# Kernel optimization log

Hardware: AMD Instinct MI355X
Metric: run time of the kernel (lower is better)

Reference implementation:

```python
import jax, jax.numpy as jnp
import numpy as np

M0, M1 = 16, 16          # n_modes
C = 64                   # hidden_channels
B = 16                   # batch
H = W = 128              # spatial resolution
SCALE = C ** (-2)        # matches torch: scale * torch.rand(...)


def setup_inputs() -> dict:
    key = jax.random.key(0)
    kx, k0r, k0i, k1r, k1i = jax.random.split(key, 5)
    X = jax.random.normal(kx, (B, C, H, W), dtype=jnp.float32)
    wshape = (C, C, M0, M1)
    # torch.rand with cfloat draws U[0,1) for real and imag parts independently
    w0r = SCALE * jax.random.uniform(k0r, wshape, dtype=jnp.float32)
    w0i = SCALE * jax.random.uniform(k0i, wshape, dtype=jnp.float32)
    w1r = SCALE * jax.random.uniform(k1r, wshape, dtype=jnp.float32)
    w1i = SCALE * jax.random.uniform(k1i, wshape, dtype=jnp.float32)
    return {"X": X, "w0r": w0r, "w0i": w0i, "w1r": w1r, "w1i": w1i}


def reference(X, w0r, w0i, w1r, w1i):
    w0 = w0r + 1j * w0i                       # linear0: (C, C, M0, M1) complex
    w1 = w1r + 1j * w1i                       # linear1
    Xf = jnp.fft.rfftn(X, axes=(-2, -1), norm="forward")   # (B, C, H, W//2+1) complex
    # out[b,c] = sum_t weight[c,t] * Xf[b,t] on the two kept-mode corners
    top = jnp.einsum("ctxy,btxy->bcxy", w0, Xf[:, :, :M0, :M1])
    bot = jnp.einsum("ctxy,btxy->bcxy", w1, Xf[:, :, -M0:, :M1])
    Y = jnp.zeros_like(Xf)
    Y = Y.at[:, :, :M0, :M1].set(top)
    Y = Y.at[:, :, -M0:, :M1].set(bot)
    out = jnp.fft.irfftn(Y, axes=(-2, -1), s=(H, W), norm="forward")
    return out.astype(jnp.float32)
```

## Files before the change

kernel.cpp:

```cpp
#include <hip/hip_runtime.h>

#define PI2 6.28318530717958647692f

__global__ __launch_bounds__(256, 4) void k_fwd(const float* __restrict__ X,
                                                float* __restrict__ Xf) {
  __shared__ __attribute__((aligned(16))) float A2t[128 * 18 * 2];
  __shared__ __attribute__((aligned(16))) float Tt[64 * 16 * 2];
  const int plane = blockIdx.x;
  const int tid = threadIdx.x;
  const float* Xp = X + (size_t)plane * (128 * 128);

  #pragma unroll
  for (int k = 0; k < 4; ++k) {
    int idx = tid + k * 256;
    int h = idx >> 4, slot = idx & 15;
    int kx = slot ? slot : 16;
    float ang = -PI2 * (float)((kx * h) & 127) / 128.f;
    float s_, c_;
    __sincosf(ang, &s_, &c_);
    Tt[idx * 2] = c_; Tt[idx * 2 + 1] = s_;
  }
  __syncthreads();

  {
    const int w2 = tid & 63;
    const int kxq = tid >> 6;
    float ar[4][2], ai[4][2];
    #pragma unroll
    for (int j = 0; j < 4; ++j) {
      ar[j][0] = 0.f; ar[j][1] = 0.f; ai[j][0] = 0.f; ai[j][1] = 0.f;
    }
    float dcA = 0.f, dcB = 0.f;
    float x0a = Xp[w2],      x1a = Xp[64 * 128 + w2];
    float x0b = Xp[w2 + 64], x1b = Xp[64 * 128 + w2 + 64];
    for (int h = 0; h < 64; ++h) {
      float n0a = 0.f, n1a = 0.f, n0b = 0.f, n1b = 0.f;
      if (h < 63) {
        n0a = Xp[(h + 1) * 128 + w2];      n1a = Xp[(h + 65) * 128 + w2];
        n0b = Xp[(h + 1) * 128 + w2 + 64]; n1b = Xp[(h + 65) * 128 + w2 + 64];
      }
      float uea = x0a + x1a, uoa = x0a - x1a;
      float ueb = x0b + x1b, uob = x0b - x1b;
      const float4* Trow = (const float4*)&Tt[h * 32];
      float4 e01 = Trow[kxq * 2];
      float4 e23 = Trow[kxq * 2 + 1];
      ar[0][0] = fmaf(uea, e01.x, ar[0][0]); ai[0][0] = fmaf(uea, e01.y, ai[0][0]);
      ar[0][1] = fmaf(ueb, e01.x, ar[0][1]); ai[0][1] = fmaf(ueb, e01.y, ai[0][1]);
      ar[1][0] = fmaf(uoa, e01.z, ar[1][0]); ai[1][0] = fmaf(uoa, e01.w, ai[1][0]);
      ar[1][1] = fmaf(uob, e01.z, ar[1][1]); ai[1][1] = fmaf(uob, e01.w, ai[1][1]);
      ar[2][0] = fmaf(uea, e23.x, ar[2][0]); ai[2][0] = fmaf(uea, e23.y, ai[2][0]);
      ar[2][1] = fmaf(ueb, e23.x, ar[2][1]); ai[2][1] = fmaf(ueb, e23.y, ai[2][1]);
      ar[3][0] = fmaf(uoa, e23.z, ar[3][0]); ai[3][0] = fmaf(uoa, e23.w, ai[3][0]);
      ar[3][1] = fmaf(uob, e23.z, ar[3][1]); ai[3][1] = fmaf(uob, e23.w, ai[3][1]);
      if (kxq == 0) { dcA += uea; dcB += ueb; }
      x0a = n0a; x1a = n1a; x0b = n0b; x1b = n1b;
    }
    #pragma unroll
    for (int j = 0; j < 4; ++j) {
      int s = kxq * 4 + j;
      int row = (s == 0) ? 16 : s;
      *(float2*)&A2t[(w2 * 18 + row) * 2]        = make_float2(ar[j][0], ai[j][0]);
      *(float2*)&A2t[((w2 + 64) * 18 + row) * 2] = make_float2(ar[j][1], ai[j][1]);
    }
    if (kxq == 0) {
      *(float2*)&A2t[(w2 * 18) * 2]        = make_float2(dcA, 0.f);
      *(float2*)&A2t[((w2 + 64) * 18) * 2] = make_float2(dcB, 0.f);
    }
  }
  __syncthreads();

  {
    const int kxi = tid >> 3;
    const int t = tid & 7;
    const int row = (kxi < 16) ? kxi : (32 - kxi);
    const float csign = (kxi < 16) ? 1.f : -1.f;
    const float s = (t & 1) ? -1.f : 1.f;
    float s0r, s0i, s1r, s1i;
    __sincosf(-PI2 * (float)t / 128.f, &s0i, &s0r);
    __sincosf(-PI2 * (float)(t + 8) / 128.f, &s1i, &s1r);
    float r0 = 0.f, i0 = 0.f, r1 = 0.f, i1 = 0.f;
    float E0r = 1.f, E0i = 0.f, E1r = 1.f, E1i = 0.f;
    #pragma unroll
    for (int half = 0; half < 2; ++half) {
      if (half == 1) {
        float c_, s_;
        __sincosf(-1.57079632679489662f * (float)t, &s_, &c_);
        E0r = c_; E0i = s_; E1r = c_; E1i = s_;
      }
      for (int w = half * 32; w < half * 32 + 32; ++w) {
        float2 a = *(const float2*)&A2t[(w * 18 + row) * 2];
        float2 b = *(const float2*)&A2t[((w + 64) * 18 + row) * 2];
        float ur = fmaf(s, b.x, a.x);
        float ui = csign * fmaf(s, b.y, a.y);
        r0 = fmaf(ur, E0r, r0); r0 = fmaf(-ui, E0i, r0);
        i0 = fmaf(ur, E0i, i0); i0 = fmaf(ui, E0r, i0);
        r1 = fmaf(ur, E1r, r1); r1 = fmaf(-ui, E1i, r1);
        i1 = fmaf(ur, E1i, i1); i1 = fmaf(ui, E1r, i1);
        float u0 = E0r * s0r - E0i * s0i; E0i = E0r * s0i + E0i * s0r; E0r = u0;
        float u1 = E1r * s1r - E1i * s1i; E1i = E1r * s1i + E1i * s1r; E1r = u1;
      }
    }
    const float sc = 1.f / 16384.f;
    float* base = Xf + (size_t)plane * 1024 + kxi * 32;
    *(float2*)&base[t * 2]       = make_float2(r0 * sc, i0 * sc);
    *(float2*)&base[(t + 8) * 2] = make_float2(r1 * sc, i1 * sc);
  }
}

__global__ __launch_bounds__(256, 2) void k_mix(const float* __restrict__ Xf,
                                                const float* __restrict__ w0r,
                                                const float* __restrict__ w0i,
                                                const float* __restrict__ w1r,
                                                const float* __restrict__ w1i,
                                                float* __restrict__ Y) {
  __shared__ __attribute__((aligned(16))) float Wl[4 * 32 * 16 * 4];
  const int bid = blockIdx.x;
  const int c2 = bid >> 8;
  const int x  = (bid >> 4) & 15;
  const int cg = bid & 15;
  const int c0 = cg * 4;
  const int kxi = c2 * 16 + x;
  const float* Wr_g = c2 ? w1r : w0r;
  const float* Wi_g = c2 ? w1i : w0i;
  const int tid = threadIdx.x;
  const int b = tid >> 4;
  const int y = tid & 15;

  #pragma unroll
  for (int k = 0; k < 16; ++k) {
    int idx = tid + k * 256;
    int y_ = idx & 15, t_ = (idx >> 4) & 63, c_ = idx >> 10;
    size_t ga = (((size_t)(c0 + c_) * 64 + t_) * 16 + x) * 16 + y_;
    int f2i = ((c_ * 32 + (t_ >> 1)) * 16 + y_) * 2 + (t_ & 1);
    *(float2*)&Wl[f2i * 2] = make_float2(Wr_g[ga], Wi_g[ga]);
  }
  __syncthreads();

  float aR[4] = {}, aI[4] = {};
  const float* xbase = Xf + ((size_t)b * 64) * 1024 + kxi * 32 + y * 2;
  for (int t8 = 0; t8 < 64; t8 += 8) {
    float2 xv[8];
    #pragma unroll
    for (int q = 0; q < 8; ++q)
      xv[q] = *(const float2*)&xbase[(size_t)(t8 + q) * 1024];
    #pragma unroll
    for (int p = 0; p < 4; ++p) {
      int t2 = (t8 >> 1) + p;
      float2 xe = xv[2 * p], xo = xv[2 * p + 1];
      #pragma unroll
      for (int cj = 0; cj < 4; ++cj) {
        float4 wv = *(const float4*)&Wl[((cj * 32 + t2) * 16 + y) * 4];
        aR[cj] = fmaf(xe.x, wv.x, aR[cj]); aR[cj] = fmaf(-xe.y, wv.y, aR[cj]);
        aI[cj] = fmaf(xe.x, wv.y, aI[cj]); aI[cj] = fmaf(xe.y, wv.x, aI[cj]);
        aR[cj] = fmaf(xo.x, wv.z, aR[cj]); aR[cj] = fmaf(-xo.y, wv.w, aR[cj]);
        aI[cj] = fmaf(xo.x, wv.w, aI[cj]); aI[cj] = fmaf(xo.y, wv.z, aI[cj]);
      }
    }
  }
  #pragma unroll
  for (int cj = 0; cj < 4; ++cj) {
    size_t ya = ((size_t)(b * 64 + c0 + cj)) * 1024 + kxi * 32 + y * 2;
    *(float2*)&Y[ya] = make_float2(aR[cj], aI[cj]);
  }
}

__global__ __launch_bounds__(256, 4) void k_inv(const float* __restrict__ Y,
                                                float* __restrict__ out) {
  __shared__ __attribute__((aligned(16))) float Yl[1024];
  __shared__ __attribute__((aligned(16))) float Mt[128 * 16 * 2];
  const int plane = blockIdx.x;
  const int tid = threadIdx.x;
  *(float4*)&Yl[tid * 4] = *(const float4*)&Y[(size_t)plane * 1024 + tid * 4];
  __syncthreads();

  {
    const int g = tid >> 6;
    const int h2 = tid & 63;
    float zr[2][4] = {}, zi[2][4] = {};
    float uw, uwi;
    __sincosf(PI2 * (float)h2 / 128.f, &uwi, &uw);
    const float4* Yl4 = (const float4*)Yl;
    float Tr = 1.f, Ti = 0.f;
    #pragma unroll 2
    for (int kxi = 0; kxi < 16; ++kxi) {
      float sgn = (kxi & 1) ? -1.f : 1.f;
      #pragma unroll
      for (int q = 0; q < 2; ++q) {
        float4 p = Yl4[kxi * 8 + g * 2 + q];
        float cr0 = p.x * Tr - p.y * Ti, ci0 = p.x * Ti + p.y * Tr;
        float cr1 = p.z * Tr - p.w * Ti, ci1 = p.z * Ti + p.w * Tr;
        zr[0][2*q]   += cr0; zi[0][2*q]   += ci0;
        zr[0][2*q+1] += cr1; zi[0][2*q+1] += ci1;
        zr[1][2*q]   = fmaf(sgn, cr0, zr[1][2*q]);   zi[1][2*q]   = fmaf(sgn, ci0, zi[1][2*q]);
        zr[1][2*q+1] = fmaf(sgn, cr1, zr[1][2*q+1]); zi[1][2*q+1] = fmaf(sgn, ci1, zi[1][2*q+1]);
      }
      float nr = Tr * uw - Ti * uwi, ni = Tr * uwi + Ti * uw;
      Tr = nr; Ti = ni;
    }
    __sincosf(PI2 * (float)((112 * h2) & 127) / 128.f, &Ti, &Tr);
    #pragma unroll 2
    for (int kxi = 16; kxi < 32; ++kxi) {
      float sgn = (kxi & 1) ? -1.f : 1.f;
      #pragma unroll
      for (int q = 0; q < 2; ++q) {
        float4 p = Yl4[kxi * 8 + g * 2 + q];
        float cr0 = p.x * Tr - p.y * Ti, ci0 = p.x * Ti + p.y * Tr;
        float cr1 = p.z * Tr - p.w * Ti, ci1 = p.z * Ti + p.w * Tr;
        zr[0][2*q]   += cr0; zi[0][2*q]   += ci0;
        zr[0][2*q+1] += cr1; zi[0][2*q+1] += ci1;
        zr[1][2*q]   = fmaf(sgn, cr0, zr[1][2*q]);   zi[1][2*q]   = fmaf(sgn, ci0, zi[1][2*q]);
        zr[1][2*q+1] = fmaf(sgn, cr1, zr[1][2*q+1]); zi[1][2*q+1] = fmaf(sgn, ci1, zi[1][2*q+1]);
      }
      float nr = Tr * uw - Ti * uwi, ni = Tr * uwi + Ti * uw;
      Tr = nr; Ti = ni;
    }
    #pragma unroll
    for (int hs = 0; hs < 2; ++hs) {
      int h = h2 + hs * 64;
      #pragma unroll
      for (int q = 0; q < 2; ++q) {
        int ky0 = g * 4 + 2 * q;
        float f0 = (ky0 == 0) ? 1.f : 2.f;
        float4 v = make_float4(f0 * zr[hs][2*q],   -f0 * zi[hs][2*q],
                               2.f * zr[hs][2*q+1], -2.f * zi[hs][2*q+1]);
        int f4i = h * 8 + ((g * 2 + q) ^ (h & 7));
        *(float4*)&Mt[f4i * 4] = v;
      }
    }
  }
  __syncthreads();

  {
    const int hp = tid >> 5;
    const int w2 = tid & 31;
    float C[16], S[16];
    {
      float cw, sw;
      __sincosf(PI2 * (float)w2 / 128.f, &sw, &cw);
      C[0] = 1.f; S[0] = 0.f;
      #pragma unroll
      for (int k = 1; k < 16; ++k) {
        C[k] = C[k - 1] * cw - S[k - 1] * sw;
        S[k] = C[k - 1] * sw + S[k - 1] * cw;
      }
    }
    float* op = out + (size_t)plane * (128 * 128);
    const float4* Mt4 = (const float4*)Mt;
    #pragma unroll 2
    for (int hj = 0; hj < 16; ++hj) {
      int h = hp * 16 + hj;
      float e = 0.f, o = 0.f, e2 = 0.f, o2 = 0.f;
      #pragma unroll
      for (int j = 0; j < 8; ++j) {
        float4 m = Mt4[h * 8 + (j ^ (h & 7))];
        int k0 = 2 * j, k1 = 2 * j + 1;
        e = fmaf(m.x, C[k0], e); e = fmaf(m.y, S[k0], e);
        o = fmaf(m.z, C[k1], o); o = fmaf(m.w, S[k1], o);
        if ((k0 & 2) == 0) { e2 = fmaf(m.x, C[k0], e2); e2 = fmaf(m.y, S[k0], e2); }
        else               { e2 = fmaf(-m.x, C[k0], e2); e2 = fmaf(-m.y, S[k0], e2); }
        if ((k1 & 2) == 0) { o2 = fmaf(m.w, C[k1], o2); o2 = fmaf(-m.z, S[k1], o2); }
        else               { o2 = fmaf(-m.w, C[k1], o2); o2 = fmaf(m.z, S[k1], o2); }
      }
      op[h * 128 + w2]      = e + o;
      op[h * 128 + w2 + 64] = e - o;
      op[h * 128 + w2 + 32] = e2 + o2;
      op[h * 128 + w2 + 96] = e2 - o2;
    }
  }
}

extern "C" void kernel_launch(void* const* d_in, const int* in_sizes, int n_in,
                              void* d_out, int out_size, void* d_ws, size_t ws_size,
                              hipStream_t stream) {
  const float* X   = (const float*)d_in[0];
  const float* w0r = (const float*)d_in[1];
  const float* w0i = (const float*)d_in[2];
  const float* w1r = (const float*)d_in[3];
  const float* w1i = (const float*)d_in[4];
  float* outp = (float*)d_out;
  float* Xf = (float*)d_ws;
  float* Yw = (float*)d_ws + (1u << 20);
  k_fwd<<<1024, 256, 0, stream>>>(X, Xf);
  k_mix<<<512, 256, 0, stream>>>(Xf, w0r, w0i, w1r, w1i, Yw);
  k_inv<<<1024, 256, 0, stream>>>(Yw, outp);
}
```

Before: 165.7 us.

## Vectorize forward-column loads and split mix kernel across more blocks

In the forward kernel, each thread now reads two adjacent columns with float2 loads, two rows per iteration, so loads are wider and more are in flight. The mix kernel grid is doubled: each block handles half the batch, and each thread handles two output channels instead of four. Weight staging now uses float4 global loads that are interleaved into shared memory. The aim is more parallelism and better memory efficiency in the mix stage, at the cost of loading each block's weight slice twice across the two batch halves.

```diff
diff --git a/kernel.cpp b/kernel.cpp
--- a/kernel.cpp
+++ b/kernel.cpp
@@ -30,41 +30,54 @@
     for (int j = 0; j < 4; ++j) {
       ar[j][0] = 0.f; ar[j][1] = 0.f; ai[j][0] = 0.f; ai[j][1] = 0.f;
     }
-    float dcA = 0.f, dcB = 0.f;
-    float x0a = Xp[w2],      x1a = Xp[64 * 128 + w2];
-    float x0b = Xp[w2 + 64], x1b = Xp[64 * 128 + w2 + 64];
-    for (int h = 0; h < 64; ++h) {
-      float n0a = 0.f, n1a = 0.f, n0b = 0.f, n1b = 0.f;
-      if (h < 63) {
-        n0a = Xp[(h + 1) * 128 + w2];      n1a = Xp[(h + 65) * 128 + w2];
-        n0b = Xp[(h + 1) * 128 + w2 + 64]; n1b = Xp[(h + 65) * 128 + w2 + 64];
-      }
-      float uea = x0a + x1a, uoa = x0a - x1a;
-      float ueb = x0b + x1b, uob = x0b - x1b;
-      const float4* Trow = (const float4*)&Tt[h * 32];
+    float dc0 = 0.f, dc1 = 0.f;
+    const float* colp = Xp + 2 * w2;
+
+    float2 t0 = *(const float2*)&colp[0];
+    float2 b0 = *(const float2*)&colp[64 * 128];
+    float2 t1 = *(const float2*)&colp[128];
+    float2 b1 = *(const float2*)&colp[65 * 128];
+
+    auto rowstep = [&](int hh, float2 tt, float2 bb) {
+      float uex = tt.x + bb.x, uox = tt.x - bb.x;
+      float uey = tt.y + bb.y, uoy = tt.y - bb.y;
+      const float4* Trow = (const float4*)&Tt[hh * 32];
       float4 e01 = Trow[kxq * 2];
       float4 e23 = Trow[kxq * 2 + 1];
-      ar[0][0] = fmaf(uea, e01.x, ar[0][0]); ai[0][0] = fmaf(uea, e01.y, ai[0][0]);
-      ar[0][1] = fmaf(ueb, e01.x, ar[0][1]); ai[0][1] = fmaf(ueb, e01.y, ai[0][1]);
-      ar[1][0] = fmaf(uoa, e01.z, ar[1][0]); ai[1][0] = fmaf(uoa, e01.w, ai[1][0]);
-      ar[1][1] = fmaf(uob, e01.z, ar[1][1]); ai[1][1] = fmaf(uob, e01.w, ai[1][1]);
-      ar[2][0] = fmaf(uea, e23.x, ar[2][0]); ai[2][0] = fmaf(uea, e23.y, ai[2][0]);
-      ar[2][1] = fmaf(ueb, e23.x, ar[2][1]); ai[2][1] = fmaf(ueb, e23.y, ai[2][1]);
-      ar[3][0] = fmaf(uoa, e23.z, ar[3][0]); ai[3][0] = fmaf(uoa, e23.w, ai[3][0]);
-      ar[3][1] = fmaf(uob, e23.z, ar[3][1]); ai[3][1] = fmaf(uob, e23.w, ai[3][1]);
-      if (kxq == 0) { dcA += uea; dcB += ueb; }
-      x0a = n0a; x1a = n1a; x0b = n0b; x1b = n1b;
-    }
+      ar[0][0] = fmaf(uex, e01.x, ar[0][0]); ai[0][0] = fmaf(uex, e01.y, ai[0][0]);
+      ar[0][1] = fmaf(uey, e01.x, ar[0][1]); ai[0][1] = fmaf(uey, e01.y, ai[0][1]);
+      ar[1][0] = fmaf(uox, e01.z, ar[1][0]); ai[1][0] = fmaf(uox, e01.w, ai[1][0]);
+      ar[1][1] = fmaf(uoy, e01.z, ar[1][1]); ai[1][1] = fmaf(uoy, e01.w, ai[1][1]);
+      ar[2][0] = fmaf(uex, e23.x, ar[2][0]); ai[2][0] = fmaf(uex, e23.y, ai[2][0]);
+      ar[2][1] = fmaf(uey, e23.x, ar[2][1]); ai[2][1] = fmaf(uey, e23.y, ai[2][1]);
+      ar[3][0] = fmaf(uox, e23.z, ar[3][0]); ai[3][0] = fmaf(uox, e23.w, ai[3][0]);
+      ar[3][1] = fmaf(uoy, e23.z, ar[3][1]); ai[3][1] = fmaf(uoy, e23.w, ai[3][1]);
+      if (kxq == 0) { dc0 += uex; dc1 += uey; }
+    };
+
+    for (int h = 0; h < 64; h += 2) {
+      float2 nt0 = make_float2(0.f, 0.f), nb0 = nt0, nt1 = nt0, nb1 = nt0;
+      if (h < 62) {
+        nt0 = *(const float2*)&colp[(h + 2) * 128];
+        nb0 = *(const float2*)&colp[(h + 66) * 128];
+        nt1 = *(const float2*)&colp[(h + 3) * 128];
+        nb1 = *(const float2*)&colp[(h + 67) * 128];
+      }
+      rowstep(h, t0, b0);
+      rowstep(h + 1, t1, b1);
+      t0 = nt0; b0 = nb0; t1 = nt1; b1 = nb1;
+    }
+
     #pragma unroll
     for (int j = 0; j < 4; ++j) {
       int s = kxq * 4 + j;
       int row = (s == 0) ? 16 : s;
-      *(float2*)&A2t[(w2 * 18 + row) * 2]        = make_float2(ar[j][0], ai[j][0]);
-      *(float2*)&A2t[((w2 + 64) * 18 + row) * 2] = make_float2(ar[j][1], ai[j][1]);
+      *(float2*)&A2t[((2 * w2) * 18 + row) * 2]     = make_float2(ar[j][0], ai[j][0]);
+      *(float2*)&A2t[((2 * w2 + 1) * 18 + row) * 2] = make_float2(ar[j][1], ai[j][1]);
     }
     if (kxq == 0) {
-      *(float2*)&A2t[(w2 * 18) * 2]        = make_float2(dcA, 0.f);
-      *(float2*)&A2t[((w2 + 64) * 18) * 2] = make_float2(dcB, 0.f);
+      *(float2*)&A2t[((2 * w2) * 18) * 2]     = make_float2(dc0, 0.f);
+      *(float2*)&A2t[((2 * w2 + 1) * 18) * 2] = make_float2(dc1, 0.f);
     }
   }
   __syncthreads();
@@ -107,7 +120,7 @@
   }
 }
 
-__global__ __launch_bounds__(256, 2) void k_mix(const float* __restrict__ Xf,
+__global__ __launch_bounds__(256, 4) void k_mix(const float* __restrict__ Xf,
                                                 const float* __restrict__ w0r,
                                                 const float* __restrict__ w0i,
                                                 const float* __restrict__ w1r,
@@ -115,28 +128,40 @@
                                                 float* __restrict__ Y) {
   __shared__ __attribute__((aligned(16))) float Wl[4 * 32 * 16 * 4];
   const int bid = blockIdx.x;
-  const int c2 = bid >> 8;
-  const int x  = (bid >> 4) & 15;
-  const int cg = bid & 15;
+  const int c2 = bid >> 9;
+  const int x  = (bid >> 5) & 15;
+  const int cg = (bid >> 1) & 15;
+  const int bh = bid & 1;
   const int c0 = cg * 4;
   const int kxi = c2 * 16 + x;
   const float* Wr_g = c2 ? w1r : w0r;
   const float* Wi_g = c2 ? w1i : w0i;
   const int tid = threadIdx.x;
-  const int b = tid >> 4;
-  const int y = tid & 15;
 
   #pragma unroll
-  for (int k = 0; k < 16; ++k) {
-    int idx = tid + k * 256;
-    int y_ = idx & 15, t_ = (idx >> 4) & 63, c_ = idx >> 10;
-    size_t ga = (((size_t)(c0 + c_) * 64 + t_) * 16 + x) * 16 + y_;
-    int f2i = ((c_ * 32 + (t_ >> 1)) * 16 + y_) * 2 + (t_ & 1);
-    *(float2*)&Wl[f2i * 2] = make_float2(Wr_g[ga], Wi_g[ga]);
-  }
-  __syncthreads();
-
-  float aR[4] = {}, aI[4] = {};
+  for (int q = 0; q < 2; ++q) {
+    int lin = tid + q * 256;
+    int y4 = lin & 3, t2 = (lin >> 2) & 31, c_ = lin >> 7;
+    size_t gae = (((size_t)(c0 + c_) * 64 + 2 * t2) * 16 + x) * 16 + y4 * 4;
+    size_t gao = gae + 256;
+    float4 wre = *(const float4*)&Wr_g[gae];
+    float4 wie = *(const float4*)&Wi_g[gae];
+    float4 wro = *(const float4*)&Wr_g[gao];
+    float4 wio = *(const float4*)&Wi_g[gao];
+    float* dst = &Wl[((c_ * 32 + t2) * 16 + y4 * 4) * 4];
+    *(float4*)&dst[0]  = make_float4(wre.x, wie.x, wro.x, wio.x);
+    *(float4*)&dst[4]  = make_float4(wre.y, wie.y, wro.y, wio.y);
+    *(float4*)&dst[8]  = make_float4(wre.z, wie.z, wro.z, wio.z);
+    *(float4*)&dst[12] = make_float4(wre.w, wie.w, wro.w, wio.w);
+  }
+  __syncthreads();
+
+  const int cs = tid >> 7;
+  const int bb = (tid >> 4) & 7;
+  const int y  = tid & 15;
+  const int b  = bh * 8 + bb;
+
+  float aR[2] = {}, aI[2] = {};
   const float* xbase = Xf + ((size_t)b * 64) * 1024 + kxi * 32 + y * 2;
   for (int t8 = 0; t8 < 64; t8 += 8) {
     float2 xv[8];
@@ -148,8 +173,8 @@
       int t2 = (t8 >> 1) + p;
       float2 xe = xv[2 * p], xo = xv[2 * p + 1];
       #pragma unroll
-      for (int cj = 0; cj < 4; ++cj) {
-        float4 wv = *(const float4*)&Wl[((cj * 32 + t2) * 16 + y) * 4];
+      for (int cj = 0; cj < 2; ++cj) {
+        float4 wv = *(const float4*)&Wl[(((cs * 2 + cj) * 32 + t2) * 16 + y) * 4];
         aR[cj] = fmaf(xe.x, wv.x, aR[cj]); aR[cj] = fmaf(-xe.y, wv.y, aR[cj]);
         aI[cj] = fmaf(xe.x, wv.y, aI[cj]); aI[cj] = fmaf(xe.y, wv.x, aI[cj]);
         aR[cj] = fmaf(xo.x, wv.z, aR[cj]); aR[cj] = fmaf(-xo.y, wv.w, aR[cj]);
@@ -158,8 +183,8 @@
     }
   }
   #pragma unroll
-  for (int cj = 0; cj < 4; ++cj) {
-    size_t ya = ((size_t)(b * 64 + c0 + cj)) * 1024 + kxi * 32 + y * 2;
+  for (int cj = 0; cj < 2; ++cj) {
+    size_t ya = ((size_t)(b * 64 + c0 + cs * 2 + cj)) * 1024 + kxi * 32 + y * 2;
     *(float2*)&Y[ya] = make_float2(aR[cj], aI[cj]);
   }
 }
@@ -281,6 +306,6 @@
   float* Xf = (float*)d_ws;
   float* Yw = (float*)d_ws + (1u << 20);
   k_fwd<<<1024, 256, 0, stream>>>(X, Xf);
-  k_mix<<<512, 256, 0, stream>>>(Xf, w0r, w0i, w1r, w1i, Yw);
+  k_mix<<<1024, 256, 0, stream>>>(Xf, w0r, w0i, w1r, w1i, Yw);
   k_inv<<<1024, 256, 0, stream>>>(Yw, outp);
 }
```

Result: slower. 186.7 us (+12.7%).
